# Kernel tuning notes

Measured on AMD Instinct MI355X. Metric: run time of the kernel, lower is better.

## Reference

```python
import jax, jax.numpy as jnp
import numpy as np

B, S, D, E, K = 4, 2048, 1024, 8, 2
LN_EPS = 1e-5


def setup_inputs() -> dict:
    key = jax.random.key(0)
    ks = jax.random.split(key, 8)
    s = 1.0 / np.sqrt(D)
    return {
        "x": jax.random.normal(ks[0], (B, S, D), dtype=jnp.float32),
        "noise": jax.random.normal(ks[1], (B, S, E), dtype=jnp.float32) * (1.0 / E),
        "W_route": jax.random.uniform(ks[2], (D, E), minval=-s, maxval=s, dtype=jnp.float32),
        "b_route": jax.random.uniform(ks[3], (E,), minval=-s, maxval=s, dtype=jnp.float32),
        "ln_gamma": jnp.ones((E,), dtype=jnp.float32),
        "ln_beta": jnp.zeros((E,), dtype=jnp.float32),
        "W_exp": jax.random.uniform(ks[4], (E, D, D), minval=-s, maxval=s, dtype=jnp.float32),
        "b_exp": jax.random.uniform(ks[5], (E, D), minval=-s, maxval=s, dtype=jnp.float32),
    }


def reference(x, noise, W_route, b_route, ln_gamma, ln_beta, W_exp, b_exp):
    # Routing: Linear(dim, E) -> LayerNorm(E) -> softmax, plus noise
    logits = jnp.einsum("bsd,de->bse", x, W_route) + b_route
    mu = logits.mean(axis=-1, keepdims=True)
    var = logits.var(axis=-1, keepdims=True)
    ln = (logits - mu) / jnp.sqrt(var + LN_EPS) * ln_gamma + ln_beta
    routing = jax.nn.softmax(ln, axis=-1) + noise

    topk_w, topk_i = jax.lax.top_k(routing, K)          # [B,S,K]
    topk_w = jax.nn.softmax(topk_w, axis=-1)

    # Dense all-expert compute (faithful to the naive original)
    expert_out = jnp.einsum("bsd,edf->bsef", x, W_exp) + b_exp  # [B,S,E,D]

    # Gather top-k experts per token and combine
    sel = jnp.take_along_axis(expert_out, topk_i[..., None], axis=2)  # [B,S,K,D]
    return (sel * topk_w[..., None]).sum(axis=2)
```

## Files before the change

### kernel.cpp

```cpp
#include <hip/hip_runtime.h>
#include <hip/hip_bf16.h>


typedef unsigned short u16;
typedef __bf16 bf16x8 __attribute__((ext_vector_type(8)));
typedef float floatx4 __attribute__((ext_vector_type(4)));
typedef unsigned short u16x8 __attribute__((ext_vector_type(8)));
typedef unsigned short u16x4 __attribute__((ext_vector_type(4)));

#define NTOK 8192
#define DDIM 1024
#define NEXP 8

__device__ __forceinline__ u16 f2bf(float f) {
    union { float f; unsigned int i; } c; c.f = f;
    unsigned int i = c.i;
    return (u16)((i + 0x7fffu + ((i >> 16) & 1u)) >> 16);
}

__device__ __forceinline__ void gl2l16(const u16* g, u16* l) {
    __builtin_amdgcn_global_load_lds(
        (const __attribute__((address_space(1))) unsigned int*)g,
        (__attribute__((address_space(3))) unsigned int*)l, 16, 0, 0);
}

__global__ __launch_bounds__(256) void transpose_w(const float* __restrict__ W,
                                                   u16* __restrict__ WT) {
    __shared__ float tileT[64 * 65];
    const int e = blockIdx.z, d0 = blockIdx.y * 64, f0 = blockIdx.x * 64;
    const int t = threadIdx.x;
    const float* src = W + (size_t)e * DDIM * DDIM;
    u16* dst = WT + (size_t)e * DDIM * DDIM;
    const int r = t >> 2, q = t & 3;
    const float* sp = src + (size_t)(d0 + r) * DDIM + f0 + q * 16;
#pragma unroll
    for (int j = 0; j < 4; ++j) {
        float4 v = *(const float4*)(sp + j * 4);
        int c = q * 16 + j * 4;
        tileT[(c + 0) * 65 + r] = v.x;
        tileT[(c + 1) * 65 + r] = v.y;
        tileT[(c + 2) * 65 + r] = v.z;
        tileT[(c + 3) * 65 + r] = v.w;
    }
    __syncthreads();
    const int c2 = t >> 2, dq = (t & 3) * 16;
    u16x8 o0, o1;
#pragma unroll
    for (int i = 0; i < 8; ++i) o0[i] = f2bf(tileT[c2 * 65 + dq + i]);
#pragma unroll
    for (int i = 0; i < 8; ++i) o1[i] = f2bf(tileT[c2 * 65 + dq + 8 + i]);
    u16* dp = dst + (size_t)(f0 + c2) * DDIM + d0 + dq;
    *(u16x8*)dp = o0;
    *(u16x8*)(dp + 8) = o1;
}

__global__ __launch_bounds__(256) void routing_compute(
    const float* __restrict__ x, const float* __restrict__ noise,
    const float* __restrict__ Wr, const float* __restrict__ br,
    const float* __restrict__ gamma, const float* __restrict__ beta,
    int* __restrict__ e01, float2* __restrict__ w01,
    u16* __restrict__ xb, int wxb) {
    __shared__ __align__(16) float wrT[NEXP][DDIM];
    const int t = threadIdx.x;
#pragma unroll
    for (int i = 0; i < 8; ++i) {
        int f4 = i * 256 + t;
        int d = f4 >> 1, half = (f4 & 1) * 4;
        float4 v = *(const float4*)&Wr[d * 8 + half];
        wrT[half + 0][d] = v.x; wrT[half + 1][d] = v.y;
        wrT[half + 2][d] = v.z; wrT[half + 3][d] = v.w;
    }
    __syncthreads();

    const int wave = t >> 6, lane = t & 63;
    const int tok = blockIdx.x * 4 + wave;
    const float4* xrow = (const float4*)(x + (size_t)tok * DDIM);
    u16* xbrow = xb + (size_t)tok * DDIM;
    float acc[8];
#pragma unroll
    for (int e = 0; e < 8; ++e) acc[e] = 0.f;
#pragma unroll
    for (int i = 0; i < 4; ++i) {
        int d4 = i * 64 + lane;
        float4 xv = xrow[d4];
        if (wxb) {
            u16x4 b;
            b[0] = f2bf(xv.x); b[1] = f2bf(xv.y);
            b[2] = f2bf(xv.z); b[3] = f2bf(xv.w);
            *(u16x4*)(xbrow + d4 * 4) = b;
        }
#pragma unroll
        for (int e = 0; e < 8; ++e) {
            float4 wv = *(const float4*)&wrT[e][d4 * 4];
            acc[e] += xv.x * wv.x + xv.y * wv.y + xv.z * wv.z + xv.w * wv.w;
        }
    }
#pragma unroll
    for (int off = 32; off >= 1; off >>= 1) {
#pragma unroll
        for (int e = 0; e < 8; ++e) acc[e] += __shfl_xor(acc[e], off, 64);
    }
    if (lane == 0) {
        float lg[8], mu = 0.f;
#pragma unroll
        for (int e = 0; e < 8; ++e) { lg[e] = acc[e] + br[e]; mu += lg[e]; }
        mu *= 0.125f;
        float var = 0.f;
#pragma unroll
        for (int e = 0; e < 8; ++e) { float d = lg[e] - mu; var += d * d; }
        var *= 0.125f;
        float rstd = rsqrtf(var + 1e-5f);
        float ln[8], mx = -1e30f;
#pragma unroll
        for (int e = 0; e < 8; ++e) {
            ln[e] = (lg[e] - mu) * rstd * gamma[e] + beta[e];
            mx = fmaxf(mx, ln[e]);
        }
        float s = 0.f, p[8];
#pragma unroll
        for (int e = 0; e < 8; ++e) { p[e] = expf(ln[e] - mx); s += p[e]; }
        float inv = 1.f / s, r[8];
#pragma unroll
        for (int e = 0; e < 8; ++e) r[e] = p[e] * inv + noise[(size_t)tok * 8 + e];
        int i0 = 0; float v0 = r[0];
#pragma unroll
        for (int e = 1; e < 8; ++e) if (r[e] > v0) { v0 = r[e]; i0 = e; }
        int i1 = -1; float v1 = -1e30f;
#pragma unroll
        for (int e = 0; e < 8; ++e) if (e != i0 && r[e] > v1) { v1 = r[e]; i1 = e; }
        float w0 = 1.f / (1.f + expf(v1 - v0));
        e01[tok] = i0 | (i1 << 8);
        w01[tok] = make_float2(w0, 1.f - w0);
    }
}

__global__ __launch_bounds__(256) void build_lists(
    const int* __restrict__ e01, const float2* __restrict__ w01,
    int* __restrict__ counts, int* __restrict__ list_tok, float* __restrict__ list_w) {
    const int g = blockIdx.x;
    const int slot = g >> 3, ex = g & 7;
    const int t = threadIdx.x, wave = t >> 6, lane = t & 63;
    __shared__ int wtot[4];
    int base = 0;
    for (int start = 0; start < NTOK; start += 256) {
        int tok = start + t;
        int packed = e01[tok];
        int e = slot ? ((packed >> 8) & 0xff) : (packed & 0xff);
        bool sel = (e == ex);
        unsigned long long m = __ballot(sel);
        int prefix = __popcll(m & ((1ULL << lane) - 1ULL));
        if (lane == 0) wtot[wave] = __popcll(m);
        __syncthreads();
        int wbase = 0;
#pragma unroll
        for (int wv = 0; wv < 4; ++wv) if (wv < wave) wbase += wtot[wv];
        int total = wtot[0] + wtot[1] + wtot[2] + wtot[3];
        if (sel) {
            float2 w2 = w01[tok];
            int pos = base + wbase + prefix;
            list_tok[g * NTOK + pos] = tok;
            list_w[g * NTOK + pos] = slot ? w2.y : w2.x;
        }
        base += total;
        __syncthreads();
    }
    if (t == 0) counts[g] = base;
}

__global__ __launch_bounds__(256, 3) void moe_gemm_bf16(
    const u16* __restrict__ xb, const u16* __restrict__ WT,
    const float* __restrict__ bexp, const int* __restrict__ counts,
    const int* __restrict__ list_tok, const float* __restrict__ list_w,
    float* __restrict__ out0, float* __restrict__ out1,
    int merged, int grp_base, int accum) {
    const int id = blockIdx.x;
    int e, slot, n, m;
    if (merged) {
        e = id & 7; slot = (id >> 3) & 1; n = (id >> 4) & 7; m = id >> 7;
    } else {
        e = id & 7; slot = 0; n = (id >> 3) & 7; m = id >> 6;
    }
    const int grp = merged ? ((slot << 3) | e) : (grp_base + e);
    float* const out = (merged && slot) ? out1 : out0;
    int cnt = counts[grp];
    cnt = cnt < 0 ? 0 : (cnt > NTOK ? NTOK : cnt);
    const int m0 = m * 128;
    if (m0 >= cnt) return;
    const int n0 = n * 128;

    __shared__ __align__(16) u16 A_s[128 * 64];
    __shared__ __align__(16) u16 B_s[128 * 64];
    __shared__ int tok_s[128];
    __shared__ float w_s[128];
    __shared__ float bias_s[128];

    const int t = threadIdx.x;
    if (t < 128) {
        int r = m0 + t;
        int rr = r < cnt ? r : cnt - 1;
        tok_s[t] = list_tok[grp * NTOK + rr] & (NTOK - 1);
        w_s[t] = (r < cnt) ? list_w[grp * NTOK + rr] : 0.f;
        bias_s[t] = bexp[e * DDIM + n0 + t];
    }
    __syncthreads();

    const int wave = t >> 6, lane = t & 63;
    const int sr = t >> 3, ch = t & 7;
    const u16* ag[4];
    const u16* bg[4];
#pragma unroll
    for (int s = 0; s < 4; ++s) {
        int row = s * 32 + sr;
        int cs = ((ch ^ (row & 7)) << 3);
        ag[s] = xb + (size_t)tok_s[row] * DDIM + cs;
        bg[s] = WT + ((size_t)e * DDIM + n0 + row) * DDIM + cs;
    }
    u16* const al = A_s + wave * 512;
    u16* const bl = B_s + wave * 512;

    const int wm = wave >> 1, wn = wave & 1;
    const int lm = lane & 15, kc = lane >> 4;

    floatx4 acc[4][4];
#pragma unroll
    for (int mi = 0; mi < 4; ++mi)
#pragma unroll
        for (int ni = 0; ni < 4; ++ni) acc[mi][ni] = (floatx4){0.f, 0.f, 0.f, 0.f};

    for (int kk = 0; kk < DDIM; kk += 64) {
        if (kk) __syncthreads();
#pragma unroll
        for (int s = 0; s < 4; ++s) {
            gl2l16(ag[s] + kk, al + s * 2048);
            gl2l16(bg[s] + kk, bl + s * 2048);
        }
        __syncthreads();
#pragma unroll
        for (int ks = 0; ks < 2; ++ks) {
            const int c = (((ks * 4 + kc) ^ (lm & 7)) << 3);
            bf16x8 af[4], bfr[4];
#pragma unroll
            for (int mi = 0; mi < 4; ++mi)
                af[mi] = *(const bf16x8*)&A_s[(wm * 64 + mi * 16 + lm) * 64 + c];
#pragma unroll
            for (int ni = 0; ni < 4; ++ni)
                bfr[ni] = *(const bf16x8*)&B_s[(wn * 64 + ni * 16 + lm) * 64 + c];
#pragma unroll
            for (int mi = 0; mi < 4; ++mi)
#pragma unroll
                for (int ni = 0; ni < 4; ++ni)
                    acc[mi][ni] = __builtin_amdgcn_mfma_f32_16x16x32_bf16(
                        af[mi], bfr[ni], acc[mi][ni], 0, 0, 0);
        }
    }

#pragma unroll
    for (int mi = 0; mi < 4; ++mi) {
        int rb = wm * 64 + mi * 16 + (lane >> 4) * 4;
#pragma unroll
        for (int reg = 0; reg < 4; ++reg) {
            int r = rb + reg;
            if (m0 + r < cnt) {
                size_t tok = (size_t)tok_s[r];
                float w = w_s[r];
                float* yrow = out + tok * DDIM + n0;
#pragma unroll
                for (int ni = 0; ni < 4; ++ni) {
                    int col = wn * 64 + ni * 16 + lm;
                    float v = w * (acc[mi][ni][reg] + bias_s[col]);
                    if (accum) v += yrow[col];
                    yrow[col] = v;
                }
            }
        }
    }
}

__global__ __launch_bounds__(256) void combine_add(const float* __restrict__ a,
                                                   float* __restrict__ o, int n4) {
    int stride = gridDim.x * 256;
    for (int i = blockIdx.x * 256 + threadIdx.x; i < n4; i += stride) {
        float4 va = ((const float4*)a)[i];
        float4 vo = ((float4*)o)[i];
        vo.x += va.x; vo.y += va.y; vo.z += va.z; vo.w += va.w;
        ((float4*)o)[i] = vo;
    }
}

__global__ __launch_bounds__(256) void moe_gemm_f32(
    const float* __restrict__ xf, const u16* __restrict__ WT,
    const float* __restrict__ bexp, const int* __restrict__ counts,
    const int* __restrict__ list_tok, const float* __restrict__ list_w,
    float* __restrict__ out, int grp_base, int accum) {
    const int id = blockIdx.x;
    const int e = id & 7;
    const int n = (id >> 3) & 7;
    const int m = id >> 6;
    const int grp = grp_base + e;
    int cnt = counts[grp];
    cnt = cnt < 0 ? 0 : (cnt > NTOK ? NTOK : cnt);
    const int m0 = m * 128;
    if (m0 >= cnt) return;
    const int n0 = n * 128;

    __shared__ __align__(16) u16 A_s[128 * 64];
    __shared__ __align__(16) u16 B_s[128 * 64];
    __shared__ int tok_s[128];
    __shared__ float w_s[128];
    __shared__ float bias_s[128];

    const int t = threadIdx.x;
    if (t < 128) {
        int r = m0 + t;
        int rr = r < cnt ? r : cnt - 1;
        tok_s[t] = list_tok[grp * NTOK + rr] & (NTOK - 1);
        w_s[t] = (r < cnt) ? list_w[grp * NTOK + rr] : 0.f;
        bias_s[t] = bexp[e * DDIM + n0 + t];
    }
    __syncthreads();

    const int sr = t >> 3;
    const int ch = t & 7;
    const int co = ch * 8;

    size_t arow[4];
    u16 *adst[4], *bdst[4];
#pragma unroll
    for (int s = 0; s < 4; ++s) {
        int row = s * 32 + sr;
        arow[s] = (size_t)tok_s[row] * DDIM + co;
        int cs = ((ch ^ (row & 7)) << 3);
        adst[s] = A_s + row * 64 + cs;
        bdst[s] = B_s + row * 64 + cs;
    }
    const u16* bsrc = WT + ((size_t)e * DDIM + n0 + sr) * DDIM + co;

    const int lane = t & 63, wave = t >> 6;
    const int wm = wave >> 1, wn = wave & 1;
    const int lm = lane & 15, kc = lane >> 4;

    floatx4 acc[4][4];
#pragma unroll
    for (int mi = 0; mi < 4; ++mi)
#pragma unroll
        for (int ni = 0; ni < 4; ++ni) acc[mi][ni] = (floatx4){0.f, 0.f, 0.f, 0.f};

    u16x8 pb[4];
    float4 pfa[4][2];
#pragma unroll
    for (int s = 0; s < 4; ++s) {
        pfa[s][0] = *(const float4*)(xf + arow[s]);
        pfa[s][1] = *(const float4*)(xf + arow[s] + 4);
        pb[s] = *(const u16x8*)(bsrc + (size_t)s * 32 * DDIM);
    }

    for (int kk = 0; kk < DDIM; kk += 64) {
        u16x8 wa[4];
#pragma unroll
        for (int s = 0; s < 4; ++s) {
            wa[s][0] = f2bf(pfa[s][0].x); wa[s][1] = f2bf(pfa[s][0].y);
            wa[s][2] = f2bf(pfa[s][0].z); wa[s][3] = f2bf(pfa[s][0].w);
            wa[s][4] = f2bf(pfa[s][1].x); wa[s][5] = f2bf(pfa[s][1].y);
            wa[s][6] = f2bf(pfa[s][1].z); wa[s][7] = f2bf(pfa[s][1].w);
        }
        __syncthreads();
#pragma unroll
        for (int s = 0; s < 4; ++s) {
            *(u16x8*)adst[s] = wa[s];
            *(u16x8*)bdst[s] = pb[s];
        }
        __syncthreads();
        const int nk = kk + 64;
        if (nk < DDIM) {
#pragma unroll
            for (int s = 0; s < 4; ++s) {
                pfa[s][0] = *(const float4*)(xf + arow[s] + nk);
                pfa[s][1] = *(const float4*)(xf + arow[s] + nk + 4);
                pb[s] = *(const u16x8*)(bsrc + (size_t)s * 32 * DDIM + nk);
            }
        }
#pragma unroll
        for (int ks = 0; ks < 2; ++ks) {
            bf16x8 af[4], bfr[4];
#pragma unroll
            for (int mi = 0; mi < 4; ++mi) {
                int row = wm * 64 + mi * 16 + lm;
                int c = (((ks * 4 + kc) ^ (row & 7)) << 3);
                af[mi] = *(const bf16x8*)&A_s[row * 64 + c];
            }
#pragma unroll
            for (int ni = 0; ni < 4; ++ni) {
                int row = wn * 64 + ni * 16 + lm;
                int c = (((ks * 4 + kc) ^ (row & 7)) << 3);
                bfr[ni] = *(const bf16x8*)&B_s[row * 64 + c];
            }
#pragma unroll
            for (int mi = 0; mi < 4; ++mi)
#pragma unroll
                for (int ni = 0; ni < 4; ++ni)
                    acc[mi][ni] = __builtin_amdgcn_mfma_f32_16x16x32_bf16(
                        af[mi], bfr[ni], acc[mi][ni], 0, 0, 0);
        }
    }

#pragma unroll
    for (int mi = 0; mi < 4; ++mi) {
        int rb = wm * 64 + mi * 16 + (lane >> 4) * 4;
#pragma unroll
        for (int reg = 0; reg < 4; ++reg) {
            int r = rb + reg;
            if (m0 + r < cnt) {
                size_t tok = (size_t)tok_s[r];
                float w = w_s[r];
                float* yrow = out + tok * DDIM + n0;
#pragma unroll
                for (int ni = 0; ni < 4; ++ni) {
                    int col = wn * 64 + ni * 16 + lm;
                    float v = w * (acc[mi][ni][reg] + bias_s[col]);
                    if (accum) v += yrow[col];
                    yrow[col] = v;
                }
            }
        }
    }
}

extern "C" void kernel_launch(void* const* d_in, const int* in_sizes, int n_in,
                              void* d_out, int out_size, void* d_ws, size_t ws_size,
                              hipStream_t stream) {
    const float* x     = (const float*)d_in[0];
    const float* noise = (const float*)d_in[1];
    const float* Wr    = (const float*)d_in[2];
    const float* br    = (const float*)d_in[3];
    const float* gamma = (const float*)d_in[4];
    const float* beta  = (const float*)d_in[5];
    const float* Wexp  = (const float*)d_in[6];
    const float* bexp  = (const float*)d_in[7];
    float* out = (float*)d_out;

    unsigned char* ws = (unsigned char*)d_ws;
    u16* WT       = (u16*)ws;
    int* counts   = (int*)(ws + 16777216);
    int* list_tok = (int*)(ws + 16777472);
    float* list_w = (float*)(ws + 17301760);
    int* e01      = (int*)(ws + 17826048);
    float2* w01   = (float2*)(ws + 17858816);
    u16* xb       = (u16*)(ws + 17924352);
    float* out1   = (float*)(ws + 34701568);
    const size_t need_bf16   = 34701568;
    const size_t need_merged = 34701568 + 33554432;

    const int have_bf16 = ws_size >= need_bf16;

    routing_compute<<<NTOK / 4, 256, 0, stream>>>(x, noise, Wr, br, gamma, beta,
                                                  e01, w01, xb, have_bf16);
    build_lists<<<16, 256, 0, stream>>>(e01, w01, counts, list_tok, list_w);
    transpose_w<<<dim3(16, 16, 8), 256, 0, stream>>>(Wexp, WT);

    if (ws_size >= need_merged) {
        moe_gemm_bf16<<<dim3(8192), 256, 0, stream>>>(
            xb, WT, bexp, counts, list_tok, list_w, out, out1, 1, 0, 0);
        combine_add<<<2048, 256, 0, stream>>>(out1, out, NTOK * DDIM / 4);
    } else if (have_bf16) {
        moe_gemm_bf16<<<dim3(4096), 256, 0, stream>>>(
            xb, WT, bexp, counts, list_tok, list_w, out, out, 0, 0, 0);
        moe_gemm_bf16<<<dim3(4096), 256, 0, stream>>>(
            xb, WT, bexp, counts, list_tok, list_w, out, out, 0, 8, 1);
    } else {
        moe_gemm_f32<<<dim3(4096), 256, 0, stream>>>(
            x, WT, bexp, counts, list_tok, list_w, out, 0, 0);
        moe_gemm_f32<<<dim3(4096), 256, 0, stream>>>(
            x, WT, bexp, counts, list_tok, list_w, out, 8, 1);
    }
}
```

Measured before the change: 213.2 us.

## Double-buffer LDS tiles in MoE GEMM and drop merged slot path

The bf16 expert GEMM now double-buffers its A and B LDS tiles. The next K-slice is loaded directly into LDS while MFMAs run on the current slice, so only one barrier per iteration remains. The merged single-launch variant with its extra output buffer and combine_add pass is removed, so the two slots always run as two sequential launches with accumulation. LDS per block doubles and occupancy drops to 2 blocks per CU, and build_lists prefetches the next chunk of e01.

```diff
diff --git a/kernel.cpp b/kernel.cpp
--- a/kernel.cpp
+++ b/kernel.cpp
@@ -142,9 +142,10 @@
     const int t = threadIdx.x, wave = t >> 6, lane = t & 63;
     __shared__ int wtot[4];
     int base = 0;
+    int packed = e01[t];
     for (int start = 0; start < NTOK; start += 256) {
+        int nxt = (start + 256 < NTOK) ? e01[start + 256 + t] : 0;
         int tok = start + t;
-        int packed = e01[tok];
         int e = slot ? ((packed >> 8) & 0xff) : (packed & 0xff);
         bool sel = (e == ex);
         unsigned long long m = __ballot(sel);
@@ -163,33 +164,29 @@
         }
         base += total;
         __syncthreads();
+        packed = nxt;
     }
     if (t == 0) counts[g] = base;
 }
 
-__global__ __launch_bounds__(256, 3) void moe_gemm_bf16(
+__global__ __launch_bounds__(256, 2) void moe_gemm_bf16(
     const u16* __restrict__ xb, const u16* __restrict__ WT,
     const float* __restrict__ bexp, const int* __restrict__ counts,
     const int* __restrict__ list_tok, const float* __restrict__ list_w,
-    float* __restrict__ out0, float* __restrict__ out1,
-    int merged, int grp_base, int accum) {
+    float* __restrict__ out, int grp_base, int accum) {
     const int id = blockIdx.x;
-    int e, slot, n, m;
-    if (merged) {
-        e = id & 7; slot = (id >> 3) & 1; n = (id >> 4) & 7; m = id >> 7;
-    } else {
-        e = id & 7; slot = 0; n = (id >> 3) & 7; m = id >> 6;
-    }
-    const int grp = merged ? ((slot << 3) | e) : (grp_base + e);
-    float* const out = (merged && slot) ? out1 : out0;
+    const int e = id & 7;
+    const int n = (id >> 3) & 7;
+    const int m = id >> 6;
+    const int grp = grp_base + e;
     int cnt = counts[grp];
     cnt = cnt < 0 ? 0 : (cnt > NTOK ? NTOK : cnt);
     const int m0 = m * 128;
     if (m0 >= cnt) return;
     const int n0 = n * 128;
 
-    __shared__ __align__(16) u16 A_s[128 * 64];
-    __shared__ __align__(16) u16 B_s[128 * 64];
+    __shared__ __align__(16) u16 A_s[2][128 * 64];
+    __shared__ __align__(16) u16 B_s[2][128 * 64];
     __shared__ int tok_s[128];
     __shared__ float w_s[128];
     __shared__ float bias_s[128];
@@ -215,8 +212,7 @@
         ag[s] = xb + (size_t)tok_s[row] * DDIM + cs;
         bg[s] = WT + ((size_t)e * DDIM + n0 + row) * DDIM + cs;
     }
-    u16* const al = A_s + wave * 512;
-    u16* const bl = B_s + wave * 512;
+    const int wof = wave * 512;
 
     const int wm = wave >> 1, wn = wave & 1;
     const int lm = lane & 15, kc = lane >> 4;
@@ -227,30 +223,46 @@
 #pragma unroll
         for (int ni = 0; ni < 4; ++ni) acc[mi][ni] = (floatx4){0.f, 0.f, 0.f, 0.f};
 
+#pragma unroll
+    for (int s = 0; s < 4; ++s) {
+        gl2l16(ag[s], &A_s[0][wof + s * 2048]);
+        gl2l16(bg[s], &B_s[0][wof + s * 2048]);
+    }
+    __syncthreads();
+
+    u16* Ar = &A_s[0][0]; u16* Br = &B_s[0][0];
+    u16* Aw = &A_s[1][0]; u16* Bw = &B_s[1][0];
+
     for (int kk = 0; kk < DDIM; kk += 64) {
-        if (kk) __syncthreads();
-#pragma unroll
-        for (int s = 0; s < 4; ++s) {
-            gl2l16(ag[s] + kk, al + s * 2048);
-            gl2l16(bg[s] + kk, bl + s * 2048);
-        }
-        __syncthreads();
+        const int nk = kk + 64;
+        if (nk < DDIM) {
+#pragma unroll
+            for (int s = 0; s < 4; ++s) {
+                gl2l16(ag[s] + nk, Aw + wof + s * 2048);
+                gl2l16(bg[s] + nk, Bw + wof + s * 2048);
+            }
+        }
 #pragma unroll
         for (int ks = 0; ks < 2; ++ks) {
             const int c = (((ks * 4 + kc) ^ (lm & 7)) << 3);
             bf16x8 af[4], bfr[4];
 #pragma unroll
             for (int mi = 0; mi < 4; ++mi)
-                af[mi] = *(const bf16x8*)&A_s[(wm * 64 + mi * 16 + lm) * 64 + c];
+                af[mi] = *(const bf16x8*)&Ar[(wm * 64 + mi * 16 + lm) * 64 + c];
 #pragma unroll
             for (int ni = 0; ni < 4; ++ni)
-                bfr[ni] = *(const bf16x8*)&B_s[(wn * 64 + ni * 16 + lm) * 64 + c];
+                bfr[ni] = *(const bf16x8*)&Br[(wn * 64 + ni * 16 + lm) * 64 + c];
 #pragma unroll
             for (int mi = 0; mi < 4; ++mi)
 #pragma unroll
                 for (int ni = 0; ni < 4; ++ni)
                     acc[mi][ni] = __builtin_amdgcn_mfma_f32_16x16x32_bf16(
                         af[mi], bfr[ni], acc[mi][ni], 0, 0, 0);
+        }
+        if (nk < DDIM) {
+            __syncthreads();
+            u16* tp = Ar; Ar = Aw; Aw = tp;
+            tp = Br; Br = Bw; Bw = tp;
         }
     }
 
@@ -273,17 +285,6 @@
                 }
             }
         }
-    }
-}
-
-__global__ __launch_bounds__(256) void combine_add(const float* __restrict__ a,
-                                                   float* __restrict__ o, int n4) {
-    int stride = gridDim.x * 256;
-    for (int i = blockIdx.x * 256 + threadIdx.x; i < n4; i += stride) {
-        float4 va = ((const float4*)a)[i];
-        float4 vo = ((float4*)o)[i];
-        vo.x += va.x; vo.y += va.y; vo.z += va.z; vo.w += va.w;
-        ((float4*)o)[i] = vo;
     }
 }
 
@@ -446,9 +447,7 @@
     int* e01      = (int*)(ws + 17826048);
     float2* w01   = (float2*)(ws + 17858816);
     u16* xb       = (u16*)(ws + 17924352);
-    float* out1   = (float*)(ws + 34701568);
-    const size_t need_bf16   = 34701568;
-    const size_t need_merged = 34701568 + 33554432;
+    const size_t need_bf16 = 34701568;
 
     const int have_bf16 = ws_size >= need_bf16;
 
@@ -457,15 +456,11 @@
     build_lists<<<16, 256, 0, stream>>>(e01, w01, counts, list_tok, list_w);
     transpose_w<<<dim3(16, 16, 8), 256, 0, stream>>>(Wexp, WT);
 
-    if (ws_size >= need_merged) {
-        moe_gemm_bf16<<<dim3(8192), 256, 0, stream>>>(
-            xb, WT, bexp, counts, list_tok, list_w, out, out1, 1, 0, 0);
-        combine_add<<<2048, 256, 0, stream>>>(out1, out, NTOK * DDIM / 4);
-    } else if (have_bf16) {
+    if (have_bf16) {
         moe_gemm_bf16<<<dim3(4096), 256, 0, stream>>>(
-            xb, WT, bexp, counts, list_tok, list_w, out, out, 0, 0, 0);
+            xb, WT, bexp, counts, list_tok, list_w, out, 0, 0);
         moe_gemm_bf16<<<dim3(4096), 256, 0, stream>>>(
-            xb, WT, bexp, counts, list_tok, list_w, out, out, 0, 8, 1);
+            xb, WT, bexp, counts, list_tok, list_w, out, 8, 1);
     } else {
         moe_gemm_f32<<<dim3(4096), 256, 0, stream>>>(
             x, WT, bexp, counts, list_tok, list_w, out, 0, 0);
```

New measurement: 227.9 us. 6.9% more time.
